# Kernel tuning notes

Hardware: AMD Instinct MI355X
Metric: run time of the kernel (lower is better)

Reference implementation:

```python
import jax, jax.numpy as jnp
import numpy as np

N = 100000   # nodes
E = 1600000  # edges (avg degree 16)
D = 128      # in_dim == hidden_dim
L = 3        # num_layers
LN_EPS = 1e-5


def setup_inputs() -> dict:
    key = jax.random.key(0)
    ks = jax.random.split(key, 4)
    x = jax.random.normal(ks[0], (N, D), dtype=jnp.float32)
    edge_index = jax.random.randint(ks[1], (2, E), 0, N, dtype=jnp.int32)
    s = 1.0 / np.sqrt(D)
    W1 = jax.random.normal(ks[2], (L, D, D), dtype=jnp.float32) * s
    b1 = jnp.zeros((L, D), jnp.float32)
    W2 = jax.random.normal(ks[3], (L, D, D), dtype=jnp.float32) * s
    b2 = jnp.zeros((L, D), jnp.float32)
    gamma = jnp.ones((L, D), jnp.float32)
    beta = jnp.zeros((L, D), jnp.float32)
    return dict(x=x, edge_index=edge_index, W1=W1, b1=b1, W2=W2, b2=b2,
                gamma=gamma, beta=beta)


def _layer_norm(h, g, b):
    mu = jnp.mean(h, axis=-1, keepdims=True)
    var = jnp.mean((h - mu) ** 2, axis=-1, keepdims=True)
    return (h - mu) * jax.lax.rsqrt(var + LN_EPS) * g + b


def reference(x, edge_index, W1, b1, W2, b2, gamma, beta):
    # PyG GINConv (eps=0): mlp(x + sum_{j in N(i)} x_j), messages flow src->dst.
    src, dst = edge_index[0], edge_index[1]
    h = x
    for l in range(L):
        agg = jax.ops.segment_sum(h[src], dst, num_segments=N)  # [N, D]
        z = h + agg                                              # (1+eps)*x + agg, eps=0
        z = jnp.maximum(z @ W1[l] + b1[l], 0.0) @ W2[l] + b2[l]  # 2-layer MLP
        h = jnp.maximum(_layer_norm(z, gamma[l], beta[l]), 0.0)  # LayerNorm + ReLU
        # dropout p=0.0 (eval): identity
    return h
```

## Files before the change

### kernel.cpp

```cpp
#include <hip/hip_runtime.h>

#define NN 100000
#define EE 1600000
#define DD 128
#define LL 3

typedef float f32x4 __attribute__((ext_vector_type(4)));
typedef _Float16 f16x8 __attribute__((ext_vector_type(8)));
typedef _Float16 f16x2 __attribute__((ext_vector_type(2)));
typedef unsigned short u16;
typedef unsigned int u32;
typedef u16 u16x8 __attribute__((ext_vector_type(8)));

#define NBUCK ((NN + 255) / 256)
#define CHUNK 16384
#define NCHUNK ((EE + CHUNK - 1) / CHUNK)
#define PADMAX 768

__device__ __forceinline__ u16 f2h_bits(float f) {
    _Float16 h = (_Float16)f;
    return __builtin_bit_cast(u16, h);
}
__device__ __forceinline__ f16x2 bc16x2(u32 v) {
    return __builtin_bit_cast(f16x2, v);
}
__device__ __forceinline__ u32 f22h(float x, float y) {
    return (u32)f2h_bits(x) | ((u32)f2h_bits(y) << 16);
}


__global__ __launch_bounds__(1024) void csr_hist(const int* __restrict__ dst,
                                                 int* __restrict__ hist_g) {
    __shared__ int h[NBUCK];
    int t = threadIdx.x, c = blockIdx.x;
    for (int i = t; i < NBUCK; i += 1024) h[i] = 0;
    __syncthreads();
    int base = c * CHUNK;
    #pragma unroll
    for (int i = 0; i < CHUNK / 1024; ++i) {
        int e = base + t + i * 1024;
        if (e < EE) atomicAdd(&h[dst[e] >> 8], 1);
    }
    __syncthreads();
    for (int i = t; i < NBUCK; i += 1024) hist_g[i * NCHUNK + c] = h[i];
}

__global__ __launch_bounds__(128) void csr_scanA(int* __restrict__ hist_g,
                                                 int* __restrict__ btot) {
    __shared__ int sh[128];
    int b = blockIdx.x, t = threadIdx.x;
    int v = (t < NCHUNK) ? hist_g[b * NCHUNK + t] : 0;
    sh[t] = v; __syncthreads();
    for (int off = 1; off < 128; off <<= 1) {
        int u = (t >= off) ? sh[t - off] : 0;
        __syncthreads();
        sh[t] += u;
        __syncthreads();
    }
    if (t < NCHUNK) hist_g[b * NCHUNK + t] = sh[t] - v;
    if (t == 127) btot[b] = sh[127];
}

__global__ __launch_bounds__(512) void csr_scanB(const int* __restrict__ btot,
                                                 int* __restrict__ bbase) {
    __shared__ int sh[512];
    int t = threadIdx.x;
    int v = (t < NBUCK) ? btot[t] : 0;
    sh[t] = v; __syncthreads();
    for (int off = 1; off < 512; off <<= 1) {
        int u = (t >= off) ? sh[t - off] : 0;
        __syncthreads();
        sh[t] += u;
        __syncthreads();
    }
    if (t < NBUCK) bbase[t] = sh[t] - v;
    if (t == 0) bbase[NBUCK] = EE;
}

__global__ __launch_bounds__(1024) void csr_scatter(const int* __restrict__ src,
                                                    const int* __restrict__ dst,
                                                    const int* __restrict__ hist_g,
                                                    const int* __restrict__ bbase,
                                                    u32* __restrict__ rec) {
    __shared__ int cur[NBUCK];
    int t = threadIdx.x, c = blockIdx.x;
    for (int i = t; i < NBUCK; i += 1024) cur[i] = bbase[i] + hist_g[i * NCHUNK + c];
    __syncthreads();
    int base = c * CHUNK;
    #pragma unroll
    for (int i = 0; i < CHUNK / 1024; ++i) {
        int e = base + t + i * 1024;
        if (e < EE) {
            int d = dst[e];
            int slot = atomicAdd(&cur[d >> 8], 1);
            rec[slot] = (u32)src[e] | ((u32)(d & 255) << 17);
        }
    }
}

__global__ __launch_bounds__(256) void csr_finalize(const u32* __restrict__ rec,
                                                    const int* __restrict__ bbase,
                                                    int* __restrict__ rbeg,
                                                    int* __restrict__ rpend,
                                                    int* __restrict__ col) {
    __shared__ int cur[256];
    __shared__ int sc[256];
    int b = blockIdx.x, t = threadIdx.x;
    int base = bbase[b], tot = bbase[b + 1] - base;
    int pbase = base + b * PADMAX;
    sc[t] = 0; __syncthreads();
    for (int r = t; r < tot; r += 256) atomicAdd(&sc[rec[base + r] >> 17], 1);
    __syncthreads();
    int cnt = sc[t];
    int pcnt = (cnt + 3) & ~3;
    sc[t] = pcnt; __syncthreads();
    for (int off = 1; off < 256; off <<= 1) {
        int u = (t >= off) ? sc[t - off] : 0;
        __syncthreads();
        sc[t] += u;
        __syncthreads();
    }
    int mybeg = pbase + sc[t] - pcnt;
    cur[t] = mybeg;
    int nid = b * 256 + t;
    if (nid < NN) { rbeg[nid] = mybeg; rpend[nid] = mybeg + pcnt; }
    for (int k = cnt; k < pcnt; ++k) col[mybeg + k] = NN;
    __syncthreads();
    for (int r = t; r < tot; r += 256) {
        u32 rc = rec[base + r];
        int slot = atomicAdd(&cur[rc >> 17], 1);
        col[slot] = (int)(rc & 0x1FFFFu);
    }
}


__global__ void cvt_kernel(const float* __restrict__ x, u32* __restrict__ ha,
                           u32* __restrict__ hb) {
    int i = blockIdx.x * blockDim.x + threadIdx.x;
    if (i < NN * 32) {
        float4 v = ((const float4*)x)[i];
        ha[i * 2]     = f22h(v.x, v.y);
        ha[i * 2 + 1] = f22h(v.z, v.w);
    } else {
        int k = i - NN * 32;
        if (k < 64) {
            ha[(size_t)NN * 64 + k] = 0;
            hb[(size_t)NN * 64 + k] = 0;
        }
    }
}


__global__ __launch_bounds__(256) void wconv_kernel(const float* __restrict__ W1,
                                                    const float* __restrict__ W2,
                                                    u16* __restrict__ img) {
    int tt = blockIdx.x * 256 + threadIdx.x;
    if (tt >= 6 * 2048) return;
    int m = tt >> 11;
    int q = tt & 2047;
    int l = m >> 1;
    const float* W = ((m & 1) ? W2 : W1) + (size_t)l * DD * DD;
    int c = q & 127;
    int k0 = (q >> 7) << 3;
    u16x8 t;
    #pragma unroll
    for (int j = 0; j < 8; ++j) t[j] = f2h_bits(W[(k0 + j) * 128 + c]);
    u32 off = ((((u32)c << 7) + k0) << 1) ^ (((u32)c & 7) << 4);
    *(u16x8*)((unsigned char*)img + (size_t)m * 32768 + off) = t;
}


__global__ __launch_bounds__(256) void agg16_kernel(
    const u32* __restrict__ h, const int* __restrict__ rbeg,
    const int* __restrict__ rpend, const int* __restrict__ col,
    u32* __restrict__ z) {
    int node = blockIdx.x * 4 + (threadIdx.x >> 6);
    int c = threadIdx.x & 63;
    const u32* hp = h + c;
    f16x2 self = bc16x2(hp[(size_t)node * 64]);
    float accx = (float)self[0], accy = (float)self[1];
    int beg = rbeg[node], end = rpend[node];
    int j = beg;
    for (; j + 8 <= end; j += 8) {
        u32 v[8];
        #pragma unroll
        for (int q = 0; q < 8; ++q) v[q] = hp[(size_t)col[j + q] * 64];
        f16x2 s0 = bc16x2(v[0]) + bc16x2(v[1]);
        f16x2 s1 = bc16x2(v[2]) + bc16x2(v[3]);
        f16x2 s2 = bc16x2(v[4]) + bc16x2(v[5]);
        f16x2 s3 = bc16x2(v[6]) + bc16x2(v[7]);
        s0 = s0 + s1; s2 = s2 + s3; s0 = s0 + s2;
        accx += (float)s0[0]; accy += (float)s0[1];
    }
    if (j < end) {
        u32 v0 = hp[(size_t)col[j] * 64];
        u32 v1 = hp[(size_t)col[j + 1] * 64];
        u32 v2 = hp[(size_t)col[j + 2] * 64];
        u32 v3 = hp[(size_t)col[j + 3] * 64];
        f16x2 t0 = bc16x2(v0) + bc16x2(v1);
        f16x2 t1 = bc16x2(v2) + bc16x2(v3);
        t0 = t0 + t1;
        accx += (float)t0[0]; accy += (float)t0[1];
    }
    z[(size_t)node * 64 + c] = f22h(accx, accy);
}


__device__ __forceinline__ void stage_img64(const u32* __restrict__ img,
                                            unsigned char* lds, int tid) {
    #pragma unroll
    for (int i = 0; i < 8; ++i) {
        int b = tid * 16 + i * 8192;
        *(uint4*)(lds + b) = *(const uint4*)((const unsigned char*)img + b);
    }
}

__global__ __launch_bounds__(512, 4) void mlp_kernel(
    const u16* __restrict__ z16, const u32* __restrict__ imgpair,
    const float* __restrict__ b1v, const float* __restrict__ b2v,
    const float* __restrict__ gam, const float* __restrict__ bet,
    u16* __restrict__ h16out, float* __restrict__ f32out)
{
    __shared__ __align__(16) unsigned char lds[65536];
    const int tid = threadIdx.x;
    const int lane = tid & 63;
    const int w = tid >> 6;
    const int rl = lane & 15;
    const int kg = lane >> 4;
    const int tile = blockIdx.x * 128;
    const int r0 = tile + w * 16;

    stage_img64(imgpair, lds, tid);

    int zrow = r0 + rl; if (zrow > NN - 1) zrow = NN - 1;
    const u16* zp = z16 + (size_t)zrow * 128;
    f16x8 afr[4];
    #pragma unroll
    for (int kt = 0; kt < 4; ++kt)
        afr[kt] = *(const f16x8*)(zp + kt * 32 + kg * 8);
    __syncthreads();

    f32x4 acc1[8];
    #pragma unroll
    for (int nt = 0; nt < 8; ++nt) {
        f32x4 acc = {0.f, 0.f, 0.f, 0.f};
        int c = nt * 16 + rl;
        #pragma unroll
        for (int kt = 0; kt < 4; ++kt) {
            int kb = kt * 32 + kg * 8;
            u32 off = ((((u32)c << 7) + kb) << 1) ^ (((u32)c & 7) << 4);
            f16x8 b = *(const f16x8*)(lds + off);
            acc = __builtin_amdgcn_mfma_f32_16x16x32_f16(afr[kt], b, acc, 0, 0, 0);
        }
        acc1[nt] = acc;
    }

    __syncthreads();

    #pragma unroll
    for (int nt = 0; nt < 8; ++nt) {
        int c = nt * 16 + rl;
        float bias = b1v[c];
        #pragma unroll
        for (int r = 0; r < 4; ++r) {
            float v = acc1[nt][r] + bias;
            v = v > 0.f ? v : 0.f;
            int fullrow = w * 16 + kg * 4 + r;
            u32 hoff = (((((u32)fullrow << 7) + c) << 1) ^ (((u32)fullrow & 7) << 4));
            *(u16*)(lds + hoff) = f2h_bits(v);
        }
    }

    f16x8 afr2[4];
    int hrow = w * 16 + rl;
    #pragma unroll
    for (int kt = 0; kt < 4; ++kt) {
        int kb = kt * 32 + kg * 8;
        u32 off = (((((u32)hrow << 7) + kb) << 1) ^ (((u32)hrow & 7) << 4));
        afr2[kt] = *(const f16x8*)(lds + off);
    }

    f32x4 acc2[8];
    #pragma unroll
    for (int nt = 0; nt < 8; ++nt) {
        f32x4 acc = {0.f, 0.f, 0.f, 0.f};
        int c = nt * 16 + rl;
        #pragma unroll
        for (int kt = 0; kt < 4; ++kt) {
            int kb = kt * 32 + kg * 8;
            u32 off = 32768u + (((((u32)c << 7) + kb) << 1) ^ (((u32)c & 7) << 4));
            f16x8 b = *(const f16x8*)(lds + off);
            acc = __builtin_amdgcn_mfma_f32_16x16x32_f16(afr2[kt], b, acc, 0, 0, 0);
        }
        float bias = b2v[c];
        acc[0] += bias; acc[1] += bias; acc[2] += bias; acc[3] += bias;
        acc2[nt] = acc;
    }

    float gamv[8], betv[8];
    #pragma unroll
    for (int nt = 0; nt < 8; ++nt) { gamv[nt] = gam[nt * 16 + rl]; betv[nt] = bet[nt * 16 + rl]; }
    #pragma unroll
    for (int r = 0; r < 4; ++r) {
        float s1 = 0.f, s2 = 0.f;
        #pragma unroll
        for (int nt = 0; nt < 8; ++nt) { float v = acc2[nt][r]; s1 += v; s2 += v * v; }
        #pragma unroll
        for (int m = 1; m < 16; m <<= 1) {
            s1 += __shfl_xor(s1, m, 64);
            s2 += __shfl_xor(s2, m, 64);
        }
        float mu = s1 * (1.f / 128.f);
        float var = s2 * (1.f / 128.f) - mu * mu;
        float rstd = rsqrtf(var + 1e-5f);
        int fullrow = r0 + kg * 4 + r;
        if (fullrow < NN) {
            #pragma unroll
            for (int nt = 0; nt < 8; ++nt) {
                float v = (acc2[nt][r] - mu) * rstd * gamv[nt] + betv[nt];
                v = v > 0.f ? v : 0.f;
                if (h16out) h16out[(size_t)fullrow * 128 + nt * 16 + rl] = f2h_bits(v);
                if (f32out) f32out[(size_t)fullrow * 128 + nt * 16 + rl] = v;
            }
        }
    }
}


extern "C" void kernel_launch(void* const* d_in, const int* in_sizes, int n_in,
                              void* d_out, int out_size, void* d_ws, size_t ws_size,
                              hipStream_t stream) {
    const float* x     = (const float*)d_in[0];
    const int*   ei    = (const int*)d_in[1];
    const float* W1    = (const float*)d_in[2];
    const float* b1    = (const float*)d_in[3];
    const float* W2    = (const float*)d_in[4];
    const float* b2    = (const float*)d_in[5];
    const float* gamma = (const float*)d_in[6];
    const float* beta  = (const float*)d_in[7];
    float* out = (float*)d_out;

    const int* src = ei;
    const int* dst = ei + EE;

    unsigned char* ws = (unsigned char*)d_ws;
    size_t off = 0;
    int* hist_g  = (int*)(ws + off); off += (size_t)NBUCK * NCHUNK * 4;
    int* btot    = (int*)(ws + off); off += (size_t)(NBUCK + 1) * 4;
    int* bbase   = (int*)(ws + off); off += (size_t)(NBUCK + 1) * 4;
    int* rbeg    = (int*)(ws + off); off += (size_t)NN * 4;
    int* rpend   = (int*)(ws + off); off += (size_t)NN * 4; off = (off + 255) & ~(size_t)255;
    u16* wimg    = (u16*)(ws + off); off += (size_t)6 * 16384 * 2; off = (off + 255) & ~(size_t)255;
    u32* rec     = (u32*)(ws + off); off += (size_t)EE * 4; off = (off + 255) & ~(size_t)255;
    int* colv    = (int*)(ws + off); off += ((size_t)EE + (size_t)NBUCK * PADMAX + 64) * 4;
    off = (off + 255) & ~(size_t)255;
    u32* h16a    = (u32*)(ws + off); off += (size_t)(NN + 1) * 64 * 4;
    u32* h16b    = (u32*)(ws + off); off += (size_t)(NN + 1) * 64 * 4;
    u32* z16     = (u32*)(ws + off); off += (size_t)NN * 64 * 4;

    csr_hist<<<NCHUNK, 1024, 0, stream>>>(dst, hist_g);
    csr_scanA<<<NBUCK, 128, 0, stream>>>(hist_g, btot);
    csr_scanB<<<1, 512, 0, stream>>>(btot, bbase);
    csr_scatter<<<NCHUNK, 1024, 0, stream>>>(src, dst, hist_g, bbase, rec);
    csr_finalize<<<NBUCK, 256, 0, stream>>>(rec, bbase, rbeg, rpend, colv);
    wconv_kernel<<<48, 256, 0, stream>>>(W1, W2, wimg);
    cvt_kernel<<<NN * 32 / 256 + 1, 256, 0, stream>>>(x, h16a, h16b);

    const u32* hin = h16a;
    u32* hnext = h16b;
    for (int l = 0; l < LL; ++l) {
        agg16_kernel<<<NN / 4, 256, 0, stream>>>(hin, rbeg, rpend, colv, z16);
        mlp_kernel<<<(NN + 127) / 128, 512, 0, stream>>>(
            (const u16*)z16,
            (const u32*)(wimg + (size_t)(2 * l) * 16384),
            b1 + l * DD, b2 + l * DD,
            gamma + l * DD, beta + l * DD,
            (l < LL - 1) ? (u16*)hnext : (u16*)nullptr,
            (l == LL - 1) ? out : (float*)nullptr);
        hin = hnext;
        hnext = (hnext == h16a) ? h16b : h16a;
    }
}
```

Baseline: 309.7 us.

## Fuse histogram, weight and input conversion into one prologue; unroll gather by 16

Merges the CSR histogram, weight fp16 conversion and input fp16 conversion into a single block-specialized launch, removing two kernel launches and letting independent work overlap. The aggregation kernel reads row bounds via readfirstlane, making them scalar, and unrolls the neighbor gather to 16 loads in flight, with an 8-wide and 4-wide tail. The cost is more registers per thread in the gather and a larger prologue grid that uses 1024-thread blocks even for the simple conversion work.

```diff
diff --git a/kernel.cpp b/kernel.cpp
--- a/kernel.cpp
+++ b/kernel.cpp
@@ -17,6 +17,9 @@
 #define NCHUNK ((EE + CHUNK - 1) / CHUNK)
 #define PADMAX 768
 
+#define WCONV_BLKS 12
+#define CVT_BLKS   3126
+
 __device__ __forceinline__ u16 f2h_bits(float f) {
     _Float16 h = (_Float16)f;
     return __builtin_bit_cast(u16, h);
@@ -29,21 +32,54 @@
 }
 
 
-__global__ __launch_bounds__(1024) void csr_hist(const int* __restrict__ dst,
-                                                 int* __restrict__ hist_g) {
+__global__ __launch_bounds__(1024) void prologue_kernel(
+    const int* __restrict__ dst, int* __restrict__ hist_g,
+    const float* __restrict__ W1, const float* __restrict__ W2, u16* __restrict__ img,
+    const float* __restrict__ x, u32* __restrict__ ha, u32* __restrict__ hb) {
     __shared__ int h[NBUCK];
-    int t = threadIdx.x, c = blockIdx.x;
-    for (int i = t; i < NBUCK; i += 1024) h[i] = 0;
-    __syncthreads();
-    int base = c * CHUNK;
-    #pragma unroll
-    for (int i = 0; i < CHUNK / 1024; ++i) {
-        int e = base + t + i * 1024;
-        if (e < EE) atomicAdd(&h[dst[e] >> 8], 1);
-    }
-    __syncthreads();
-    for (int i = t; i < NBUCK; i += 1024) hist_g[i * NCHUNK + c] = h[i];
-}
+    int b = blockIdx.x, t = threadIdx.x;
+    if (b < NCHUNK) {
+        for (int i = t; i < NBUCK; i += 1024) h[i] = 0;
+        __syncthreads();
+        int base = b * CHUNK;
+        #pragma unroll
+        for (int i = 0; i < CHUNK / 1024; ++i) {
+            int e = base + t + i * 1024;
+            if (e < EE) atomicAdd(&h[dst[e] >> 8], 1);
+        }
+        __syncthreads();
+        for (int i = t; i < NBUCK; i += 1024) hist_g[i * NCHUNK + b] = h[i];
+    } else if (b < NCHUNK + WCONV_BLKS) {
+        int tt = (b - NCHUNK) * 1024 + t;
+        if (tt < 6 * 2048) {
+            int m = tt >> 11;
+            int q = tt & 2047;
+            int l = m >> 1;
+            const float* W = ((m & 1) ? W2 : W1) + (size_t)l * DD * DD;
+            int c = q & 127;
+            int k0 = (q >> 7) << 3;
+            u16x8 tv;
+            #pragma unroll
+            for (int j = 0; j < 8; ++j) tv[j] = f2h_bits(W[(k0 + j) * 128 + c]);
+            u32 off = ((((u32)c << 7) + k0) << 1) ^ (((u32)c & 7) << 4);
+            *(u16x8*)((unsigned char*)img + (size_t)m * 32768 + off) = tv;
+        }
+    } else {
+        int i = (b - NCHUNK - WCONV_BLKS) * 1024 + t;
+        if (i < NN * 32) {
+            float4 v = ((const float4*)x)[i];
+            ha[i * 2]     = f22h(v.x, v.y);
+            ha[i * 2 + 1] = f22h(v.z, v.w);
+        } else {
+            int k = i - NN * 32;
+            if (k < 64) {
+                ha[(size_t)NN * 64 + k] = 0;
+                hb[(size_t)NN * 64 + k] = 0;
+            }
+        }
+    }
+}
+
 
 __global__ __launch_bounds__(128) void csr_scanA(int* __restrict__ hist_g,
                                                  int* __restrict__ btot) {
@@ -134,42 +170,6 @@
 }
 
 
-__global__ void cvt_kernel(const float* __restrict__ x, u32* __restrict__ ha,
-                           u32* __restrict__ hb) {
-    int i = blockIdx.x * blockDim.x + threadIdx.x;
-    if (i < NN * 32) {
-        float4 v = ((const float4*)x)[i];
-        ha[i * 2]     = f22h(v.x, v.y);
-        ha[i * 2 + 1] = f22h(v.z, v.w);
-    } else {
-        int k = i - NN * 32;
-        if (k < 64) {
-            ha[(size_t)NN * 64 + k] = 0;
-            hb[(size_t)NN * 64 + k] = 0;
-        }
-    }
-}
-
-
-__global__ __launch_bounds__(256) void wconv_kernel(const float* __restrict__ W1,
-                                                    const float* __restrict__ W2,
-                                                    u16* __restrict__ img) {
-    int tt = blockIdx.x * 256 + threadIdx.x;
-    if (tt >= 6 * 2048) return;
-    int m = tt >> 11;
-    int q = tt & 2047;
-    int l = m >> 1;
-    const float* W = ((m & 1) ? W2 : W1) + (size_t)l * DD * DD;
-    int c = q & 127;
-    int k0 = (q >> 7) << 3;
-    u16x8 t;
-    #pragma unroll
-    for (int j = 0; j < 8; ++j) t[j] = f2h_bits(W[(k0 + j) * 128 + c]);
-    u32 off = ((((u32)c << 7) + k0) << 1) ^ (((u32)c & 7) << 4);
-    *(u16x8*)((unsigned char*)img + (size_t)m * 32768 + off) = t;
-}
-
-
 __global__ __launch_bounds__(256) void agg16_kernel(
     const u32* __restrict__ h, const int* __restrict__ rbeg,
     const int* __restrict__ rpend, const int* __restrict__ col,
@@ -179,9 +179,27 @@
     const u32* hp = h + c;
     f16x2 self = bc16x2(hp[(size_t)node * 64]);
     float accx = (float)self[0], accy = (float)self[1];
-    int beg = rbeg[node], end = rpend[node];
+    int beg = __builtin_amdgcn_readfirstlane(rbeg[node]);
+    int end = __builtin_amdgcn_readfirstlane(rpend[node]);
     int j = beg;
-    for (; j + 8 <= end; j += 8) {
+    for (; j + 16 <= end; j += 16) {
+        u32 v[16];
+        #pragma unroll
+        for (int q = 0; q < 16; ++q) v[q] = hp[(size_t)col[j + q] * 64];
+        f16x2 s0 = bc16x2(v[0]) + bc16x2(v[1]);
+        f16x2 s1 = bc16x2(v[2]) + bc16x2(v[3]);
+        f16x2 s2 = bc16x2(v[4]) + bc16x2(v[5]);
+        f16x2 s3 = bc16x2(v[6]) + bc16x2(v[7]);
+        s0 = s0 + s1; s2 = s2 + s3; s0 = s0 + s2;
+        accx += (float)s0[0]; accy += (float)s0[1];
+        f16x2 s4 = bc16x2(v[8]) + bc16x2(v[9]);
+        f16x2 s5 = bc16x2(v[10]) + bc16x2(v[11]);
+        f16x2 s6 = bc16x2(v[12]) + bc16x2(v[13]);
+        f16x2 s7 = bc16x2(v[14]) + bc16x2(v[15]);
+        s4 = s4 + s5; s6 = s6 + s7; s4 = s4 + s6;
+        accx += (float)s4[0]; accy += (float)s4[1];
+    }
+    if (j + 8 <= end) {
         u32 v[8];
         #pragma unroll
         for (int q = 0; q < 8; ++q) v[q] = hp[(size_t)col[j + q] * 64];
@@ -191,6 +209,7 @@
         f16x2 s3 = bc16x2(v[6]) + bc16x2(v[7]);
         s0 = s0 + s1; s2 = s2 + s3; s0 = s0 + s2;
         accx += (float)s0[0]; accy += (float)s0[1];
+        j += 8;
     }
     if (j < end) {
         u32 v0 = hp[(size_t)col[j] * 64];
@@ -358,13 +377,12 @@
     u32* h16b    = (u32*)(ws + off); off += (size_t)(NN + 1) * 64 * 4;
     u32* z16     = (u32*)(ws + off); off += (size_t)NN * 64 * 4;
 
-    csr_hist<<<NCHUNK, 1024, 0, stream>>>(dst, hist_g);
+    prologue_kernel<<<NCHUNK + WCONV_BLKS + CVT_BLKS, 1024, 0, stream>>>(
+        dst, hist_g, W1, W2, wimg, x, h16a, h16b);
     csr_scanA<<<NBUCK, 128, 0, stream>>>(hist_g, btot);
     csr_scanB<<<1, 512, 0, stream>>>(btot, bbase);
     csr_scatter<<<NCHUNK, 1024, 0, stream>>>(src, dst, hist_g, bbase, rec);
     csr_finalize<<<NBUCK, 256, 0, stream>>>(rec, bbase, rbeg, rpend, colv);
-    wconv_kernel<<<48, 256, 0, stream>>>(W1, W2, wimg);
-    cvt_kernel<<<NN * 32 / 256 + 1, 256, 0, stream>>>(x, h16a, h16b);
 
     const u32* hin = h16a;
     u32* hnext = h16b;
```

Result: faster. 296.6 us (-4.2%).
